# Optimization experiments

Measured on AMD Instinct MI355X. Metric: run time of the kernel, lower is better.

The kernel has to match this reference:

```python
import jax, jax.numpy as jnp
import numpy as np


def setup_inputs() -> dict:
    key = jax.random.key(0)
    k1, k2 = jax.random.split(key)
    B, S, I, H = 1, 1024, 512, 64
    J = I
    a = jax.random.normal(k1, (B, S, I, H), dtype=jnp.float32)
    b = jax.random.normal(k2, (B, S, J, H), dtype=jnp.float32)
    return {"a": a, "b": b}


def reference(a, b):
    # a: [*, s, i, h], b: [*, s, j, h] -> mean_s(a_sih outer b_sjh): [*, i, j, h]
    # Equivalent to the torch code's '...ish,...jsh->...ijsh' followed by mean over s,
    # but contracted directly without materializing the [*, i, j, s, h] intermediate.
    s = a.shape[-3]
    return jnp.einsum('...sih,...sjh->...ijh', a, b) / s
```

## Files before the change

### kernel.cpp

```cpp
#include <hip/hip_runtime.h>
#include <stdint.h>

typedef float f32x4 __attribute__((ext_vector_type(4)));
typedef short bf16x8 __attribute__((ext_vector_type(8)));
typedef float fragc __attribute__((ext_vector_type(4)));
typedef uint32_t u32x4 __attribute__((ext_vector_type(4)));

__device__ __forceinline__ uint32_t pk2(float lo, float hi) {
  return __builtin_amdgcn_perm(__float_as_uint(hi), __float_as_uint(lo), 0x07060302u);
}

__device__ __forceinline__ void gload16(const void* g, void* l) {
  __builtin_amdgcn_global_load_lds((const __attribute__((address_space(1))) uint32_t*)g,
                                   (__attribute__((address_space(3))) uint32_t*)l, 16, 0, 0);
}

#define WS_B_OFF 67108864ull

__global__ __launch_bounds__(512) void pack_kernel(const float* __restrict__ Ag,
                                                   const float* __restrict__ Bg,
                                                   uint8_t* __restrict__ ws) {
  const int bid  = blockIdx.x;
  const int rw   = bid & 7;
  const int kq   = (bid >> 3) & 127;
  const int side = bid >> 10;
  const int t    = threadIdx.x;

  const f32x4* S4 = (const f32x4*)(side ? Bg : Ag);
  uint8_t* dst = ws + (side ? WS_B_OFF : 0ull);

  const int base = rw * 1024 + t;
  f32x4 r1[8], r2[8];
#pragma unroll
  for (int e = 0; e < 8; ++e) {
    r1[e] = __builtin_nontemporal_load(&S4[(size_t)(kq * 8 + e) * 8192 + base]);
    r2[e] = __builtin_nontemporal_load(&S4[(size_t)(kq * 8 + e) * 8192 + base + 512]);
  }

  const int hq = t & 15;
  const int ra = t >> 4;
#pragma unroll
  for (int e = 0; e < 4; ++e) {
    const int h = hq * 4 + e;
    u32x4 o1, o2;
    o1[0] = pk2(r1[0][e], r1[1][e]); o1[1] = pk2(r1[2][e], r1[3][e]);
    o1[2] = pk2(r1[4][e], r1[5][e]); o1[3] = pk2(r1[6][e], r1[7][e]);
    o2[0] = pk2(r2[0][e], r2[1][e]); o2[1] = pk2(r2[2][e], r2[3][e]);
    o2[2] = pk2(r2[4][e], r2[5][e]); o2[3] = pk2(r2[6][e], r2[7][e]);
    uint8_t* plane = dst + ((size_t)((kq * 8 + rw) * 64 + h)) * 1024;
    *(u32x4*)(plane + ra * 16) = o1;
    *(u32x4*)(plane + (ra + 32) * 16) = o2;
  }
}

__global__ __launch_bounds__(512, 2) void gemm_kernel(const uint8_t* __restrict__ ws,
                                                      float* __restrict__ Og) {
  __shared__ alignas(16) uint8_t lds[131072];

  const int bid = blockIdx.x;
  const int x   = bid & 7;
  const int r   = bid >> 3;
  const int ip  = (x >> 2) * 2 + (r & 1);
  const int jt  = ((x >> 1) & 1) * 2 + ((r >> 1) & 1);
  const int hg  = (x & 1) * 8 + (r >> 2);
  const int i0  = ip * 128;
  const int j0  = jt * 128;
  const int hg4 = hg * 4;

  const int t = threadIdx.x, lane = t & 63, w = t >> 6;
  const int hl = w & 3, half = w >> 2;
  const int frl = lane & 15, frg = lane >> 4;

  const uint8_t* Apk = ws;
  const uint8_t* Bpk = ws + WS_B_OFF;

  fragc acc[4][8];
#pragma unroll
  for (int m = 0; m < 4; ++m)
#pragma unroll
    for (int n = 0; n < 8; ++n)
      acc[m][n] = (fragc)0.0f;

#define ISSUE(kt, b)                                                                \
  {                                                                                 \
    _Pragma("unroll") for (int k2 = 0; k2 < 2; ++k2) {                              \
      const int ko = half * 2 + k2;                                                 \
      _Pragma("unroll") for (int p = 0; p < 2; ++p) {                               \
        const size_t pa =                                                           \
            ((size_t)(((kt) * 4 + ko) * 8 + (i0 >> 6) + p) * 64 + hg4 + hl) * 1024; \
        const size_t pb =                                                           \
            ((size_t)(((kt) * 4 + ko) * 8 + (j0 >> 6) + p) * 64 + hg4 + hl) * 1024; \
        gload16(Apk + pa + lane * 16,                                               \
                lds + (b) * 65536 + hl * 8192 + ko * 2048 + p * 1024);              \
        gload16(Bpk + pb + lane * 16,                                               \
                lds + (b) * 65536 + 32768 + hl * 8192 + ko * 2048 + p * 1024);      \
      }                                                                             \
    }                                                                               \
  }

  ISSUE(0, 0)

  for (int kt = 0; kt < 32; ++kt) {
    __syncthreads();
    const int b = kt & 1;
    if (kt < 31) ISSUE(kt + 1, b ^ 1)
    const uint8_t* La = lds + b * 65536 + hl * 8192;
    const uint8_t* Lb = La + 32768;
    bf16x8 fb[8];
#pragma unroll
    for (int n = 0; n < 8; ++n)
      fb[n] = *(const bf16x8*)(Lb + frg * 2048 + (n * 16 + frl) * 16);
#pragma unroll
    for (int m = 0; m < 4; ++m) {
      bf16x8 fa = *(const bf16x8*)(La + frg * 2048 + (half * 64 + m * 16 + frl) * 16);
#pragma unroll
      for (int n = 0; n < 8; ++n)
        acc[m][n] = __builtin_amdgcn_mfma_f32_16x16x32_bf16(fa, fb[n], acc[m][n], 0, 0, 0);
    }
  }
#undef ISSUE

  const float scale = 1.0f / 1024.0f;
  const int i_r = t >> 4, jo = t & 15;
#pragma unroll
  for (int cb = 0; cb < 4; ++cb) {
    __syncthreads();
    if (half == (cb >> 1)) {
#pragma unroll
      for (int m2 = 0; m2 < 2; ++m2) {
        const int m = (cb & 1) * 2 + m2;
#pragma unroll
        for (int n = 0; n < 8; ++n) {
#pragma unroll
          for (int q = 0; q < 4; ++q) {
            const int il = m2 * 16 + frg * 4 + q;
            const int j  = n * 16 + frl;
            int byte = (il * 128 + j) * 16 + hl * 4;
            byte ^= ((byte >> 7) & 7) << 4;
            *(float*)(lds + byte) = acc[m][n][q] * scale;
          }
        }
      }
    }
    __syncthreads();
#pragma unroll
    for (int c = 0; c < 8; ++c) {
      int byte = (i_r * 128 + jo * 8 + c) * 16;
      byte ^= ((byte >> 7) & 7) << 4;
      const f32x4 v = *(const f32x4*)(lds + byte);
      *(f32x4*)(Og + ((size_t)(i0 + cb * 32 + i_r) * 512 + (j0 + jo * 8 + c)) * 64 + hg4) = v;
    }
  }
}

extern "C" void kernel_launch(void* const* d_in, const int* in_sizes, int n_in,
                              void* d_out, int out_size, void* d_ws, size_t ws_size,
                              hipStream_t stream) {
  const float* a = (const float*)d_in[0];
  const float* b = (const float*)d_in[1];
  float* out = (float*)d_out;
  uint8_t* ws = (uint8_t*)d_ws;
  pack_kernel<<<2048, 512, 0, stream>>>(a, b, ws);
  gemm_kernel<<<256, 512, 0, stream>>>(ws, out);
}
```

Baseline: 133.9 us.

## Stage GEMM tiles through registers into single-buffered LDS, raise occupancy hint

Replaces direct global-to-LDS async loads with double-buffered LDS by register prefetch: the next k-tile is loaded into registers during the MFMA loop, then written to a single 64KB LDS buffer after a barrier. It also halves LDS use and raises the launch_bounds min-blocks from 2 to 4 to allow more resident workgroups. The pack kernel's loads and stores are split into two separate phases. The cost is an extra barrier per iteration, more VGPR pressure from the prefetch registers, and possibly spills under the tighter occupancy bound.

```diff
diff --git a/kernel.cpp b/kernel.cpp
--- a/kernel.cpp
+++ b/kernel.cpp
@@ -8,11 +8,6 @@
 
 __device__ __forceinline__ uint32_t pk2(float lo, float hi) {
   return __builtin_amdgcn_perm(__float_as_uint(hi), __float_as_uint(lo), 0x07060302u);
-}
-
-__device__ __forceinline__ void gload16(const void* g, void* l) {
-  __builtin_amdgcn_global_load_lds((const __attribute__((address_space(1))) uint32_t*)g,
-                                   (__attribute__((address_space(3))) uint32_t*)l, 16, 0, 0);
 }
 
 #define WS_B_OFF 67108864ull
@@ -32,30 +27,37 @@
   const int base = rw * 1024 + t;
   f32x4 r1[8], r2[8];
 #pragma unroll
-  for (int e = 0; e < 8; ++e) {
+  for (int e = 0; e < 8; ++e)
     r1[e] = __builtin_nontemporal_load(&S4[(size_t)(kq * 8 + e) * 8192 + base]);
+#pragma unroll
+  for (int e = 0; e < 8; ++e)
     r2[e] = __builtin_nontemporal_load(&S4[(size_t)(kq * 8 + e) * 8192 + base + 512]);
-  }
 
   const int hq = t & 15;
   const int ra = t >> 4;
 #pragma unroll
   for (int e = 0; e < 4; ++e) {
     const int h = hq * 4 + e;
-    u32x4 o1, o2;
+    u32x4 o1;
     o1[0] = pk2(r1[0][e], r1[1][e]); o1[1] = pk2(r1[2][e], r1[3][e]);
     o1[2] = pk2(r1[4][e], r1[5][e]); o1[3] = pk2(r1[6][e], r1[7][e]);
+    uint8_t* plane = dst + ((size_t)((kq * 8 + rw) * 64 + h)) * 1024;
+    *(u32x4*)(plane + ra * 16) = o1;
+  }
+#pragma unroll
+  for (int e = 0; e < 4; ++e) {
+    const int h = hq * 4 + e;
+    u32x4 o2;
     o2[0] = pk2(r2[0][e], r2[1][e]); o2[1] = pk2(r2[2][e], r2[3][e]);
     o2[2] = pk2(r2[4][e], r2[5][e]); o2[3] = pk2(r2[6][e], r2[7][e]);
     uint8_t* plane = dst + ((size_t)((kq * 8 + rw) * 64 + h)) * 1024;
-    *(u32x4*)(plane + ra * 16) = o1;
     *(u32x4*)(plane + (ra + 32) * 16) = o2;
   }
 }
 
-__global__ __launch_bounds__(512, 2) void gemm_kernel(const uint8_t* __restrict__ ws,
+__global__ __launch_bounds__(512, 4) void gemm_kernel(const uint8_t* __restrict__ ws,
                                                       float* __restrict__ Og) {
-  __shared__ alignas(16) uint8_t lds[131072];
+  __shared__ alignas(16) uint8_t lds[65536];
 
   const int bid = blockIdx.x;
   const int x   = bid & 7;
@@ -81,7 +83,9 @@
     for (int n = 0; n < 8; ++n)
       acc[m][n] = (fragc)0.0f;
 
-#define ISSUE(kt, b)                                                                \
+  f32x4 sa[4], sb[4];
+
+#define LOADR(kt)                                                                   \
   {                                                                                 \
     _Pragma("unroll") for (int k2 = 0; k2 < 2; ++k2) {                              \
       const int ko = half * 2 + k2;                                                 \
@@ -90,35 +94,53 @@
             ((size_t)(((kt) * 4 + ko) * 8 + (i0 >> 6) + p) * 64 + hg4 + hl) * 1024; \
         const size_t pb =                                                           \
             ((size_t)(((kt) * 4 + ko) * 8 + (j0 >> 6) + p) * 64 + hg4 + hl) * 1024; \
-        gload16(Apk + pa + lane * 16,                                               \
-                lds + (b) * 65536 + hl * 8192 + ko * 2048 + p * 1024);              \
-        gload16(Bpk + pb + lane * 16,                                               \
-                lds + (b) * 65536 + 32768 + hl * 8192 + ko * 2048 + p * 1024);      \
+        sa[k2 * 2 + p] = *(const f32x4*)(Apk + pa + lane * 16);                     \
+        sb[k2 * 2 + p] = *(const f32x4*)(Bpk + pb + lane * 16);                     \
       }                                                                             \
     }                                                                               \
   }
 
-  ISSUE(0, 0)
+#define WSTAGE()                                                                    \
+  {                                                                                 \
+    _Pragma("unroll") for (int k2 = 0; k2 < 2; ++k2) {                              \
+      const int ko = half * 2 + k2;                                                 \
+      _Pragma("unroll") for (int p = 0; p < 2; ++p) {                               \
+        const int lo = hl * 8192 + ko * 2048 + p * 1024 + lane * 16;                \
+        *(f32x4*)(lds + lo) = sa[k2 * 2 + p];                                       \
+        *(f32x4*)(lds + 32768 + lo) = sb[k2 * 2 + p];                               \
+      }                                                                             \
+    }                                                                               \
+  }
+
+  LOADR(0)
+  WSTAGE()
+  __syncthreads();
 
   for (int kt = 0; kt < 32; ++kt) {
-    __syncthreads();
-    const int b = kt & 1;
-    if (kt < 31) ISSUE(kt + 1, b ^ 1)
-    const uint8_t* La = lds + b * 65536 + hl * 8192;
-    const uint8_t* Lb = La + 32768;
-    bf16x8 fb[8];
-#pragma unroll
-    for (int n = 0; n < 8; ++n)
-      fb[n] = *(const bf16x8*)(Lb + frg * 2048 + (n * 16 + frl) * 16);
-#pragma unroll
-    for (int m = 0; m < 4; ++m) {
-      bf16x8 fa = *(const bf16x8*)(La + frg * 2048 + (half * 64 + m * 16 + frl) * 16);
+    if (kt < 31) LOADR(kt + 1)
+    {
+      const uint8_t* La = lds + hl * 8192;
+      const uint8_t* Lb = La + 32768;
+      bf16x8 fb[8];
 #pragma unroll
       for (int n = 0; n < 8; ++n)
-        acc[m][n] = __builtin_amdgcn_mfma_f32_16x16x32_bf16(fa, fb[n], acc[m][n], 0, 0, 0);
+        fb[n] = *(const bf16x8*)(Lb + frg * 2048 + (n * 16 + frl) * 16);
+#pragma unroll
+      for (int m = 0; m < 4; ++m) {
+        bf16x8 fa = *(const bf16x8*)(La + frg * 2048 + (half * 64 + m * 16 + frl) * 16);
+#pragma unroll
+        for (int n = 0; n < 8; ++n)
+          acc[m][n] = __builtin_amdgcn_mfma_f32_16x16x32_bf16(fa, fb[n], acc[m][n], 0, 0, 0);
+      }
+    }
+    __syncthreads();
+    if (kt < 31) {
+      WSTAGE()
+      __syncthreads();
     }
   }
-#undef ISSUE
+#undef LOADR
+#undef WSTAGE
 
   const float scale = 1.0f / 1024.0f;
   const int i_r = t >> 4, jo = t & 15;
```

After: 394.0 us. 2.94x slower.
